# Optimization experiments

Measured on AMD Instinct MI355X. Metric: run time of the kernel, lower is better.

The kernel has to match this reference:

```python
import jax, jax.numpy as jnp
import numpy as np

B, C, T, H, W = 8, 512, 8, 32, 32
CI = C // 2  # inter_channels
EPS = 1e-5


def _conv1x1(x, w, b):
    # x: (b, c, t, h, w); w: (o, c); b: (o,)
    return jnp.einsum('bcthw,oc->bothw', x, w) + b[None, :, None, None, None]


def _maxpool2(v):
    # MaxPool3d(kernel=2, stride=2) on (t, h, w)
    b, c, t, h, w = v.shape
    return v.reshape(b, c, t // 2, 2, h // 2, 2, w // 2, 2).max(axis=(3, 5, 7))


def setup_inputs() -> dict:
    key = jax.random.key(0)
    ks = jax.random.split(key, 12)
    s = 0.02
    return {
        'x': jax.random.normal(ks[0], (B, C, T, H, W), dtype=jnp.float32),
        'theta_w': jax.random.normal(ks[1], (CI, C), dtype=jnp.float32) * s,
        'theta_b': jnp.zeros((CI,), dtype=jnp.float32),
        'phi_w': jax.random.normal(ks[2], (CI, C), dtype=jnp.float32) * s,
        'phi_b': jnp.zeros((CI,), dtype=jnp.float32),
        'g_w': jax.random.normal(ks[3], (CI, C), dtype=jnp.float32) * s,
        'g_b': jnp.zeros((CI,), dtype=jnp.float32),
        'wz_w': jax.random.normal(ks[4], (C, CI), dtype=jnp.float32) * s,
        'wz_b': jnp.zeros((C,), dtype=jnp.float32),
        'bn_gamma': jax.random.uniform(ks[5], (C,), dtype=jnp.float32, minval=0.5, maxval=1.5),
        'bn_beta': jax.random.normal(ks[6], (C,), dtype=jnp.float32) * 0.1,
    }


def reference(x, theta_w, theta_b, phi_w, phi_b, g_w, g_b, wz_w, wz_b, bn_gamma, bn_beta):
    b = x.shape[0]
    # projections (1x1x1 convs == channel matmuls)
    theta_x = _conv1x1(x, theta_w, theta_b)            # (b, ci, t, h, w)
    phi_x = _maxpool2(_conv1x1(x, phi_w, phi_b))       # (b, ci, t/2, h/2, w/2)
    g_x = _maxpool2(_conv1x1(x, g_w, g_b))             # (b, ci, t/2, h/2, w/2)

    ci = theta_x.shape[1]
    q = theta_x.reshape(b, ci, -1).transpose(0, 2, 1)  # (b, N, ci)
    k = phi_x.reshape(b, ci, -1)                       # (b, ci, M)
    v = g_x.reshape(b, ci, -1).transpose(0, 2, 1)      # (b, M, ci)

    f = jnp.einsum('bnc,bcm->bnm', q, k)               # (b, N, M)
    attn = jax.nn.softmax(f, axis=-1)                  # embedded_gaussian
    y = jnp.einsum('bnm,bmc->bnc', attn, v)            # (b, N, ci)
    y = y.transpose(0, 2, 1).reshape(b, ci, *x.shape[2:])

    # Wz: 1x1x1 conv + BatchNorm3d (training-mode batch stats, eps=1e-5)
    z = _conv1x1(y, wz_w, wz_b)                        # (b, C, t, h, w)
    mean = z.mean(axis=(0, 2, 3, 4), keepdims=True)
    var = z.var(axis=(0, 2, 3, 4), keepdims=True)
    z = (z - mean) * jax.lax.rsqrt(var + EPS)
    z = z * bn_gamma[None, :, None, None, None] + bn_beta[None, :, None, None, None]
    return z + x
```

## Files before the change

kernel.cpp:

```cpp
#include <hip/hip_runtime.h>
#include <math.h>

typedef unsigned short u16;
typedef __attribute__((ext_vector_type(8))) _Float16 half8;
typedef __attribute__((ext_vector_type(4))) float f32x4;

#define NS 8192
#define MS 1024
#define CCH 512
#define CI 256
#define O3 768

__device__ __forceinline__ float h2f(u16 u) {
    _Float16 h; *(u16*)&h = u; return (float)h;
}
__device__ __forceinline__ u16 f2h(float f) {
    _Float16 h = (_Float16)f; return *(u16*)&h;
}

__device__ __forceinline__ void gld16(u16* lds, const u16* g) {
    __builtin_amdgcn_global_load_lds((const __attribute__((address_space(1))) void*)g,
                                     (__attribute__((address_space(3))) void*)lds,
                                     16, 0, 0);
}

__global__ void prep_w(const float* __restrict__ tw, const float* __restrict__ tb,
                       const float* __restrict__ pw, const float* __restrict__ pb,
                       const float* __restrict__ gw, const float* __restrict__ gb,
                       const float* __restrict__ wzw,
                       u16* __restrict__ W3b, float* __restrict__ b3, u16* __restrict__ wzb) {
    int i = blockIdx.x * 256 + threadIdx.x;
    if (i < O3 * CCH) {
        int o = i >> 9, c = i & 511;
        float v = (o < 256) ? tw[o * 512 + c] : (o < 512) ? pw[(o - 256) * 512 + c]
                                              : gw[(o - 512) * 512 + c];
        W3b[i] = f2h(v);
    } else {
        int j = i - O3 * CCH;
        if (j < CCH * CI) wzb[j] = f2h(wzw[j]);
    }
    if (i < O3) b3[i] = (i < 256) ? tb[i] : (i < 512) ? pb[i - 256] : gb[i - 512];
}

__global__ __launch_bounds__(256) void transpose_x(const float* __restrict__ x,
                                                   u16* __restrict__ xt) {
    __shared__ float tile[64][129];
    int b = blockIdx.z;
    int n0 = blockIdx.x * 128, c0 = blockIdx.y * 64;
    const float* xb = x + ((size_t)b * CCH + c0) * NS + n0;
    int t = threadIdx.x;
    #pragma unroll
    for (int i = 0; i < 32; ++i) {
        int idx = t + i * 256;
        int c = idx >> 7, n = idx & 127;
        tile[c][n] = xb[(size_t)c * NS + n];
    }
    __syncthreads();
    u16* xo = xt + ((size_t)b * NS + n0) * CCH + c0;
    #pragma unroll
    for (int i = 0; i < 16; ++i) {
        int idx = t + i * 256;
        int cp = idx & 31, n = idx >> 5;
        unsigned lo = f2h(tile[2 * cp][n]);
        unsigned hi = f2h(tile[2 * cp + 1][n]);
        *(unsigned*)(xo + (size_t)n * CCH + 2 * cp) = lo | (hi << 16);
    }
}

template<int BIAS_MODE>
__global__ __launch_bounds__(256) void gemm_nt_f16(
        const u16* __restrict__ A, const u16* __restrict__ Bm,
        u16* __restrict__ C, const float* __restrict__ bias,
        int lda, int ldb, int ldc, int Ksize,
        size_t strideA, size_t strideB, size_t strideC) {
    __shared__ u16 As[128 * 64];
    __shared__ u16 Bs[128 * 64];
    const int t = threadIdx.x;
    const int l = t & 63, w = t >> 6;
    const int wr = w >> 1, wc = w & 1;
    const int fr = l & 15, fq = l >> 4;

    const int nx = gridDim.x, ny = gridDim.y;
    int bid = blockIdx.x + nx * (blockIdx.y + ny * blockIdx.z);
    int cpx = (nx * ny * (int)gridDim.z) >> 3;
    int W = (bid & 7) * cpx + (bid >> 3);
    int bx = W % nx, rem = W / nx;
    int by = rem % ny, bz = rem / ny;

    const u16* gA = A + (size_t)bz * strideA + (size_t)(by * 128) * lda;
    const u16* gB = Bm + (size_t)bz * strideB + (size_t)(bx * 128) * ldb;

    f32x4 acc[4][4];
    #pragma unroll
    for (int m = 0; m < 4; ++m)
        #pragma unroll
        for (int n = 0; n < 4; ++n) acc[m][n] = (f32x4)0.f;

    for (int k0 = 0; k0 < Ksize; k0 += 64) {
        #pragma unroll
        for (int i = 0; i < 4; ++i) {
            int cd = t + i * 256;
            int row = cd >> 3, k8 = (cd & 7) * 8;
            int lbase = (cd & ~63) * 8;
            gld16(&As[lbase], gA + (size_t)row * lda + k0 + k8);
            gld16(&Bs[lbase], gB + (size_t)row * ldb + k0 + k8);
        }
        __syncthreads();

        half8 fa[4][2], fb[4][2];
        #pragma unroll
        for (int m = 0; m < 4; ++m)
            #pragma unroll
            for (int kk = 0; kk < 2; ++kk) {
                fa[m][kk] = *(const half8*)&As[(wr * 64 + m * 16 + fr) * 64 + kk * 32 + fq * 8];
                fb[m][kk] = *(const half8*)&Bs[(wc * 64 + m * 16 + fr) * 64 + kk * 32 + fq * 8];
            }
        #pragma unroll
        for (int kk = 0; kk < 2; ++kk)
            #pragma unroll
            for (int m = 0; m < 4; ++m)
                #pragma unroll
                for (int n = 0; n < 4; ++n)
                    acc[m][n] = __builtin_amdgcn_mfma_f32_16x16x32_f16(
                        fa[m][kk], fb[n][kk], acc[m][n], 0, 0, 0);
        __syncthreads();
    }

    u16* gC = C + (size_t)bz * strideC;
    const int crow0 = by * 128 + wr * 64;
    const int ccol0 = bx * 128 + wc * 64;
    #pragma unroll
    for (int m = 0; m < 4; ++m) {
        #pragma unroll
        for (int n = 0; n < 4; ++n) {
            int col = ccol0 + n * 16 + fr;
            float cb = (BIAS_MODE == 2) ? bias[col] : 0.f;
            #pragma unroll
            for (int j = 0; j < 4; ++j) {
                int row = crow0 + m * 16 + fq * 4 + j;
                float v = acc[m][n][j] + cb;
                if (BIAS_MODE == 1) v += bias[row];
                gC[(size_t)row * ldc + col] = f2h(v);
            }
        }
    }
}

__global__ __launch_bounds__(256) void pool_kernel(const u16* __restrict__ proj,
                                                   u16* __restrict__ kb, u16* __restrict__ vg) {
    int tid = blockIdx.x * 256 + threadIdx.x;
    int b = tid >> 18;
    int m = (tid >> 8) & 1023;
    int ci = tid & 255;
    int tp = m >> 8, hp = (m >> 4) & 15, wp = m & 15;
    const u16* pb = proj + (size_t)b * NS * O3;
    float mk = -1e30f, mv = -1e30f;
    #pragma unroll
    for (int d = 0; d < 8; ++d) {
        int dt = d >> 2, dh = (d >> 1) & 1, dw = d & 1;
        int n = (2 * tp + dt) * 1024 + (2 * hp + dh) * 32 + (2 * wp + dw);
        const u16* r = pb + (size_t)n * O3;
        mk = fmaxf(mk, h2f(r[256 + ci]));
        mv = fmaxf(mv, h2f(r[512 + ci]));
    }
    kb[((size_t)b * MS + m) * CI + ci] = f2h(mk);
    vg[((size_t)b * CI + ci) * MS + m] = f2h(mv);
}

__global__ __launch_bounds__(512, 2) void attn_fused(
        const u16* __restrict__ proj, const u16* __restrict__ kb,
        const u16* __restrict__ vg, u16* __restrict__ y) {
    __shared__ u16 Ks[2][64 * 256];
    __shared__ u16 Vs[2][256 * 64];
    __shared__ u16 Ps[8][16][40];

    int bid0 = blockIdx.x + 64 * blockIdx.y;
    int W = (bid0 & 7) * 64 + (bid0 >> 3);
    const int b = W >> 6;
    const int n0 = (W & 63) * 128;

    const int t = threadIdx.x;
    const int l = t & 63, w = t >> 6;
    const int fr = l & 15, fq = l >> 4;

    const u16* projb = proj + (size_t)b * NS * O3;
    const u16* kbb = kb + (size_t)b * MS * CI;
    const u16* vgb = vg + (size_t)b * CI * MS;

    half8 qf[8];
    {
        const u16* qrow = projb + (size_t)(n0 + w * 16 + fr) * O3 + fq * 8;
        #pragma unroll
        for (int kk = 0; kk < 8; ++kk)
            qf[kk] = *(const half8*)(qrow + kk * 32);
    }

    f32x4 accO[16];
    #pragma unroll
    for (int nf = 0; nf < 16; ++nf) accO[nf] = (f32x4)0.f;
    float m_run[4], l_run[4];
    #pragma unroll
    for (int j = 0; j < 4; ++j) { m_run[j] = -1e30f; l_run[j] = 0.f; }

    #define STAGE_KV(buf, m0)                                                     \
        {                                                                         \
            _Pragma("unroll")                                                     \
            for (int i = 0; i < 4; ++i) {                                         \
                int c = t + i * 512;                                              \
                int lb = (c & ~63) << 3;                                          \
                int krow = c >> 5, kk8 = c & 31;                                  \
                gld16(&Ks[buf][lb],                                               \
                      kbb + (size_t)((m0) + krow) * CI + ((kk8 ^ (krow & 7)) << 3)); \
                int vrow = c >> 3, vk8 = c & 7;                                   \
                gld16(&Vs[buf][lb],                                               \
                      vgb + (size_t)vrow * MS + (m0) + ((vk8 ^ (vrow & 7)) << 3)); \
            }                                                                     \
        }

    STAGE_KV(0, 0);
    STAGE_KV(1, 64);

    for (int mt = 0; mt < 16; ++mt) {
        const int cur = mt & 1;
        if (mt == 15) asm volatile("s_waitcnt vmcnt(0)" ::: "memory");
        else          asm volatile("s_waitcnt vmcnt(8)" ::: "memory");
        __builtin_amdgcn_sched_barrier(0);
        __builtin_amdgcn_s_barrier();

        f32x4 accS[4];
        #pragma unroll
        for (int nf = 0; nf < 4; ++nf) accS[nf] = (f32x4)0.f;
        __builtin_amdgcn_s_setprio(1);
        #pragma unroll
        for (int kk = 0; kk < 8; ++kk) {
            half8 fb[4];
            #pragma unroll
            for (int nf = 0; nf < 4; ++nf) {
                int row = nf * 16 + fr;
                fb[nf] = *(const half8*)&Ks[cur][row * 256 + (((kk << 2) | fq) ^ (row & 7)) * 8];
            }
            #pragma unroll
            for (int nf = 0; nf < 4; ++nf)
                accS[nf] = __builtin_amdgcn_mfma_f32_16x16x32_f16(
                    qf[kk], fb[nf], accS[nf], 0, 0, 0);
        }
        __builtin_amdgcn_s_setprio(0);

        float pm[4];
        #pragma unroll
        for (int j = 0; j < 4; ++j)
            pm[j] = fmaxf(fmaxf(accS[0][j], accS[1][j]),
                          fmaxf(accS[2][j], accS[3][j]));
        #pragma unroll
        for (int off = 1; off < 16; off <<= 1)
            #pragma unroll
            for (int j = 0; j < 4; ++j)
                pm[j] = fmaxf(pm[j], __shfl_xor(pm[j], off));

        int chg = 0;
        #pragma unroll
        for (int j = 0; j < 4; ++j) chg |= (pm[j] > m_run[j]);
        if (__any(chg)) {
            #pragma unroll
            for (int j = 0; j < 4; ++j) {
                float mn = fmaxf(m_run[j], pm[j]);
                float a = __expf(m_run[j] - mn);
                m_run[j] = mn;
                l_run[j] *= a;
                #pragma unroll
                for (int nf = 0; nf < 16; ++nf) accO[nf][j] *= a;
            }
        }

        #pragma unroll
        for (int kkm = 0; kkm < 2; ++kkm) {
            #pragma unroll
            for (int j = 0; j < 4; ++j) {
                float ps = 0.f;
                #pragma unroll
                for (int nfh = 0; nfh < 2; ++nfh) {
                    float p = __expf(accS[kkm * 2 + nfh][j] - m_run[j]);
                    ps += p;
                    Ps[w][fq * 4 + j][nfh * 16 + fr] = f2h(p);
                }
                #pragma unroll
                for (int off = 1; off < 16; off <<= 1) ps += __shfl_xor(ps, off);
                l_run[j] += ps;
            }
            half8 fa = *(const half8*)&Ps[w][fr][fq * 8];
            __builtin_amdgcn_s_setprio(1);
            #pragma unroll
            for (int nf = 0; nf < 16; ++nf) {
                int row = nf * 16 + fr;
                half8 fbv = *(const half8*)&Vs[cur][row * 64 + (((kkm << 2) | fq) ^ (row & 7)) * 8];
                accO[nf] = __builtin_amdgcn_mfma_f32_16x16x32_f16(
                    fa, fbv, accO[nf], 0, 0, 0);
            }
            __builtin_amdgcn_s_setprio(0);
        }

        __builtin_amdgcn_s_barrier();
        if (mt < 14) STAGE_KV(cur, (mt + 2) * 64);
    }

    u16* yb = y + ((size_t)b * NS + n0 + w * 16) * CI;
    #pragma unroll
    for (int j = 0; j < 4; ++j) {
        float inv = 1.f / l_run[j];
        int row = fq * 4 + j;
        #pragma unroll
        for (int nf = 0; nf < 16; ++nf)
            yb[(size_t)row * CI + nf * 16 + fr] = f2h(accO[nf][j] * inv);
    }
    #undef STAGE_KV
}

__global__ __launch_bounds__(256) void bn_stats(const u16* __restrict__ z,
                                                float* __restrict__ stats) {
    int c = blockIdx.x, t = threadIdx.x;
    float s = 0.f, q = 0.f;
    for (int b = 0; b < 8; ++b) {
        const u16* p = z + ((size_t)b * CCH + c) * NS;
        #pragma unroll
        for (int i = 0; i < 4; ++i) {
            uint4 v = *(const uint4*)(p + (t + i * 256) * 8);
            const u16* u = (const u16*)&v;
            #pragma unroll
            for (int j = 0; j < 8; ++j) { float f = h2f(u[j]); s += f; q += f * f; }
        }
    }
    #pragma unroll
    for (int off = 32; off; off >>= 1) { s += __shfl_xor(s, off); q += __shfl_xor(q, off); }
    __shared__ float rs[4], rq[4];
    int w = t >> 6;
    if ((t & 63) == 0) { rs[w] = s; rq[w] = q; }
    __syncthreads();
    if (t == 0) {
        float S2 = rs[0] + rs[1] + rs[2] + rs[3];
        float Q = rq[0] + rq[1] + rq[2] + rq[3];
        const float inv = 1.f / 65536.f;
        float mean = S2 * inv;
        float var = Q * inv - mean * mean;
        stats[c] = mean;
        stats[CCH + c] = rsqrtf(var + 1e-5f);
    }
}

__global__ __launch_bounds__(256) void bn_final(const u16* __restrict__ z,
                                                const float* __restrict__ x,
                                                const float* __restrict__ stats,
                                                const float* __restrict__ gamma,
                                                const float* __restrict__ beta,
                                                float* __restrict__ out) {
    size_t i = ((size_t)blockIdx.x * 256 + threadIdx.x) * 8;
    int c = (int)((i >> 13) & 511);
    float g = gamma[c] * stats[CCH + c];
    float sh = beta[c] - stats[c] * g;
    uint4 zv = *(const uint4*)(z + i);
    const u16* u = (const u16*)&zv;
    float4 x0 = *(const float4*)(x + i);
    float4 x1 = *(const float4*)(x + i + 4);
    float4 o0, o1;
    o0.x = h2f(u[0]) * g + sh + x0.x;
    o0.y = h2f(u[1]) * g + sh + x0.y;
    o0.z = h2f(u[2]) * g + sh + x0.z;
    o0.w = h2f(u[3]) * g + sh + x0.w;
    o1.x = h2f(u[4]) * g + sh + x1.x;
    o1.y = h2f(u[5]) * g + sh + x1.y;
    o1.z = h2f(u[6]) * g + sh + x1.z;
    o1.w = h2f(u[7]) * g + sh + x1.w;
    *(float4*)(out + i) = o0;
    *(float4*)(out + i + 4) = o1;
}

extern "C" void kernel_launch(void* const* d_in, const int* in_sizes, int n_in,
                              void* d_out, int out_size, void* d_ws, size_t ws_size,
                              hipStream_t stream) {
    const float* x       = (const float*)d_in[0];
    const float* theta_w = (const float*)d_in[1];
    const float* theta_b = (const float*)d_in[2];
    const float* phi_w   = (const float*)d_in[3];
    const float* phi_b   = (const float*)d_in[4];
    const float* g_w     = (const float*)d_in[5];
    const float* g_b     = (const float*)d_in[6];
    const float* wz_w    = (const float*)d_in[7];
    const float* wz_b    = (const float*)d_in[8];
    const float* gamma   = (const float*)d_in[9];
    const float* beta    = (const float*)d_in[10];

    char* base = (char*)d_ws;
    u16*   W3b  = (u16*)base;
    float* b3   = (float*)(base + 786432);
    u16*   wzb  = (u16*)(base + 789504);
    float* stats= (float*)(base + 1051648);
    u16* xt   = (u16*)(base + 1056768);
    u16* kb   = xt;
    u16* vg   = xt + (size_t)8 * MS * CI;
    u16* z    = xt;
    u16* proj = (u16*)(base + 1056768 + 67108864);
    u16* y    = (u16*)(base + 1056768 + 67108864 + 100663296);

    prep_w<<<2048, 256, 0, stream>>>(theta_w, theta_b, phi_w, phi_b, g_w, g_b,
                                     wz_w, W3b, b3, wzb);
    transpose_x<<<dim3(64, 8, 8), 256, 0, stream>>>(x, xt);

    gemm_nt_f16<2><<<dim3(6, 64, 8), 256, 0, stream>>>(
        xt, W3b, proj, b3, CCH, CCH, O3, CCH,
        (size_t)NS * CCH, 0, (size_t)NS * O3);

    pool_kernel<<<8192, 256, 0, stream>>>(proj, kb, vg);

    attn_fused<<<dim3(64, 8), 512, 0, stream>>>(proj, kb, vg, y);

    gemm_nt_f16<1><<<dim3(64, 4, 8), 256, 0, stream>>>(
        wzb, y, z, wz_b, CI, CI, NS, CI,
        0, (size_t)NS * CI, (size_t)CCH * NS);

    bn_stats<<<CCH, 256, 0, stream>>>(z, stats);

    bn_final<<<16384, 256, 0, stream>>>(z, x, stats, gamma, beta, (float*)d_out);
}
```

Before: 388.1 us.

## Fuse x transpose/fp16 conversion into projection GEMM and XOR-swizzle LDS tiles

```diff
diff --git a/kernel.cpp b/kernel.cpp
--- a/kernel.cpp
+++ b/kernel.cpp
@@ -42,28 +42,101 @@
     if (i < O3) b3[i] = (i < 256) ? tb[i] : (i < 512) ? pb[i - 256] : gb[i - 512];
 }
 
-__global__ __launch_bounds__(256) void transpose_x(const float* __restrict__ x,
-                                                   u16* __restrict__ xt) {
-    __shared__ float tile[64][129];
-    int b = blockIdx.z;
-    int n0 = blockIdx.x * 128, c0 = blockIdx.y * 64;
-    const float* xb = x + ((size_t)b * CCH + c0) * NS + n0;
-    int t = threadIdx.x;
-    #pragma unroll
-    for (int i = 0; i < 32; ++i) {
-        int idx = t + i * 256;
-        int c = idx >> 7, n = idx & 127;
-        tile[c][n] = xb[(size_t)c * NS + n];
-    }
-    __syncthreads();
-    u16* xo = xt + ((size_t)b * NS + n0) * CCH + c0;
-    #pragma unroll
-    for (int i = 0; i < 16; ++i) {
-        int idx = t + i * 256;
-        int cp = idx & 31, n = idx >> 5;
-        unsigned lo = f2h(tile[2 * cp][n]);
-        unsigned hi = f2h(tile[2 * cp + 1][n]);
-        *(unsigned*)(xo + (size_t)n * CCH + 2 * cp) = lo | (hi << 16);
+__global__ __launch_bounds__(256) void proj_gemm(
+        const float* __restrict__ x, const u16* __restrict__ W3b,
+        const float* __restrict__ b3, u16* __restrict__ proj) {
+    __shared__ float Traw[64][129];
+    __shared__ u16 As[128 * 64];
+    __shared__ u16 Bs[128 * 64];
+    const int t = threadIdx.x;
+    const int l = t & 63, w = t >> 6;
+    const int wr = w >> 1, wc = w & 1;
+    const int fr = l & 15, fq = l >> 4;
+
+    const int nx = gridDim.x, ny = gridDim.y;
+    int bid = blockIdx.x + nx * (blockIdx.y + ny * blockIdx.z);
+    int cpx = (nx * ny * (int)gridDim.z) >> 3;
+    int Wd = (bid & 7) * cpx + (bid >> 3);
+    int bx = Wd % nx, rem = Wd / nx;
+    int by = rem % ny, bz = rem / ny;
+
+    const float* gx = x + (size_t)bz * CCH * NS + by * 128;
+    const u16* gB = W3b + (size_t)(bx * 128) * CCH;
+
+    f32x4 acc[4][4];
+    #pragma unroll
+    for (int m = 0; m < 4; ++m)
+        #pragma unroll
+        for (int n = 0; n < 4; ++n) acc[m][n] = (f32x4)0.f;
+
+    for (int k0 = 0; k0 < CCH; k0 += 64) {
+        #pragma unroll
+        for (int i = 0; i < 4; ++i) {
+            int cd = t + i * 256;
+            int row = cd >> 3;
+            int k8 = ((cd & 7) ^ (row & 7)) * 8;
+            int lbase = (cd & ~63) * 8;
+            gld16(&Bs[lbase], gB + (size_t)row * CCH + k0 + k8);
+        }
+        #pragma unroll
+        for (int i = 0; i < 8; ++i) {
+            int idx = t + i * 256;
+            int c = idx >> 5, nq = idx & 31;
+            float4 v = *(const float4*)(gx + (size_t)(k0 + c) * NS + nq * 4);
+            Traw[c][nq * 4 + 0] = v.x;
+            Traw[c][nq * 4 + 1] = v.y;
+            Traw[c][nq * 4 + 2] = v.z;
+            Traw[c][nq * 4 + 3] = v.w;
+        }
+        __syncthreads();
+        #pragma unroll
+        for (int i = 0; i < 16; ++i) {
+            int idx = t + i * 256;
+            int cp = idx & 31, n = idx >> 5;
+            unsigned lo = f2h(Traw[2 * cp][n]);
+            unsigned hi = f2h(Traw[2 * cp + 1][n]);
+            int chunk = (cp >> 2) ^ (n & 7);
+            *(unsigned*)((char*)As + n * 128 + chunk * 16 + (cp & 3) * 4)
+                = lo | (hi << 16);
+        }
+        __syncthreads();
+
+        half8 fa[4][2], fb[4][2];
+        #pragma unroll
+        for (int m = 0; m < 4; ++m)
+            #pragma unroll
+            for (int kk = 0; kk < 2; ++kk) {
+                int ra = wr * 64 + m * 16 + fr;
+                int rb = wc * 64 + m * 16 + fr;
+                fa[m][kk] = *(const half8*)&As[ra * 64 + ((((kk << 2) | fq)) ^ (ra & 7)) * 8];
+                fb[m][kk] = *(const half8*)&Bs[rb * 64 + ((((kk << 2) | fq)) ^ (rb & 7)) * 8];
+            }
+        #pragma unroll
+        for (int kk = 0; kk < 2; ++kk)
+            #pragma unroll
+            for (int m = 0; m < 4; ++m)
+                #pragma unroll
+                for (int n = 0; n < 4; ++n)
+                    acc[m][n] = __builtin_amdgcn_mfma_f32_16x16x32_f16(
+                        fa[m][kk], fb[n][kk], acc[m][n], 0, 0, 0);
+        __syncthreads();
+    }
+
+    u16* gC = proj + (size_t)bz * NS * O3;
+    const int crow0 = by * 128 + wr * 64;
+    const int ccol0 = bx * 128 + wc * 64;
+    #pragma unroll
+    for (int m = 0; m < 4; ++m) {
+        #pragma unroll
+        for (int n = 0; n < 4; ++n) {
+            int col = ccol0 + n * 16 + fr;
+            float cb = b3[col];
+            #pragma unroll
+            for (int j = 0; j < 4; ++j) {
+                int row = crow0 + m * 16 + fq * 4 + j;
+                gC[(size_t)row * O3 + col] = f2h(acc[m][n][j] + cb);
+            }
+        }
     }
 }
 
@@ -83,8 +156,8 @@
     const int nx = gridDim.x, ny = gridDim.y;
     int bid = blockIdx.x + nx * (blockIdx.y + ny * blockIdx.z);
     int cpx = (nx * ny * (int)gridDim.z) >> 3;
-    int W = (bid & 7) * cpx + (bid >> 3);
-    int bx = W % nx, rem = W / nx;
+    int Wd = (bid & 7) * cpx + (bid >> 3);
+    int bx = Wd % nx, rem = Wd / nx;
     int by = rem % ny, bz = rem / ny;
 
     const u16* gA = A + (size_t)bz * strideA + (size_t)(by * 128) * lda;
@@ -100,7 +173,8 @@
         #pragma unroll
         for (int i = 0; i < 4; ++i) {
             int cd = t + i * 256;
-            int row = cd >> 3, k8 = (cd & 7) * 8;
+            int row = cd >> 3;
+            int k8 = ((cd & 7) ^ (row & 7)) * 8;
             int lbase = (cd & ~63) * 8;
             gld16(&As[lbase], gA + (size_t)row * lda + k0 + k8);
             gld16(&Bs[lbase], gB + (size_t)row * ldb + k0 + k8);
@@ -112,8 +186,10 @@
         for (int m = 0; m < 4; ++m)
             #pragma unroll
             for (int kk = 0; kk < 2; ++kk) {
-                fa[m][kk] = *(const half8*)&As[(wr * 64 + m * 16 + fr) * 64 + kk * 32 + fq * 8];
-                fb[m][kk] = *(const half8*)&Bs[(wc * 64 + m * 16 + fr) * 64 + kk * 32 + fq * 8];
+                int ra = wr * 64 + m * 16 + fr;
+                int rb = wc * 64 + m * 16 + fr;
+                fa[m][kk] = *(const half8*)&As[ra * 64 + ((((kk << 2) | fq)) ^ (ra & 7)) * 8];
+                fb[m][kk] = *(const half8*)&Bs[rb * 64 + ((((kk << 2) | fq)) ^ (rb & 7)) * 8];
             }
         #pragma unroll
         for (int kk = 0; kk < 2; ++kk)
@@ -393,20 +469,16 @@
     float* b3   = (float*)(base + 786432);
     u16*   wzb  = (u16*)(base + 789504);
     float* stats= (float*)(base + 1051648);
-    u16* xt   = (u16*)(base + 1056768);
-    u16* kb   = xt;
-    u16* vg   = xt + (size_t)8 * MS * CI;
-    u16* z    = xt;
+    u16* kb   = (u16*)(base + 1056768);
+    u16* vg   = kb + (size_t)8 * MS * CI;
+    u16* z    = kb;
     u16* proj = (u16*)(base + 1056768 + 67108864);
     u16* y    = (u16*)(base + 1056768 + 67108864 + 100663296);
 
     prep_w<<<2048, 256, 0, stream>>>(theta_w, theta_b, phi_w, phi_b, g_w, g_b,
                                      wz_w, W3b, b3, wzb);
-    transpose_x<<<dim3(64, 8, 8), 256, 0, stream>>>(x, xt);
-
-    gemm_nt_f16<2><<<dim3(6, 64, 8), 256, 0, stream>>>(
-        xt, W3b, proj, b3, CCH, CCH, O3, CCH,
-        (size_t)NS * CCH, 0, (size_t)NS * O3);
+
+    proj_gemm<<<dim3(6, 64, 8), 256, 0, stream>>>(x, W3b, b3, proj);
 
     pool_kernel<<<8192, 256, 0, stream>>>(proj, kb, vg);
 
```

Measured after the change: 426.5 us. 1.1x slower.

## Double-buffer GEMM LDS tiles with async prefetch and XOR swizzle

Applied to the files above, without the earlier changes.

```diff
diff --git a/kernel.cpp b/kernel.cpp
--- a/kernel.cpp
+++ b/kernel.cpp
@@ -73,8 +73,8 @@
         u16* __restrict__ C, const float* __restrict__ bias,
         int lda, int ldb, int ldc, int Ksize,
         size_t strideA, size_t strideB, size_t strideC) {
-    __shared__ u16 As[128 * 64];
-    __shared__ u16 Bs[128 * 64];
+    __shared__ u16 As[2][128 * 64];
+    __shared__ u16 Bs[2][128 * 64];
     const int t = threadIdx.x;
     const int l = t & 63, w = t >> 6;
     const int wr = w >> 1, wc = w & 1;
@@ -83,8 +83,8 @@
     const int nx = gridDim.x, ny = gridDim.y;
     int bid = blockIdx.x + nx * (blockIdx.y + ny * blockIdx.z);
     int cpx = (nx * ny * (int)gridDim.z) >> 3;
-    int W = (bid & 7) * cpx + (bid >> 3);
-    int bx = W % nx, rem = W / nx;
+    int Wd = (bid & 7) * cpx + (bid >> 3);
+    int bx = Wd % nx, rem = Wd / nx;
     int by = rem % ny, bz = rem / ny;
 
     const u16* gA = A + (size_t)bz * strideA + (size_t)(by * 128) * lda;
@@ -96,25 +96,41 @@
         #pragma unroll
         for (int n = 0; n < 4; ++n) acc[m][n] = (f32x4)0.f;
 
-    for (int k0 = 0; k0 < Ksize; k0 += 64) {
-        #pragma unroll
-        for (int i = 0; i < 4; ++i) {
-            int cd = t + i * 256;
-            int row = cd >> 3, k8 = (cd & 7) * 8;
-            int lbase = (cd & ~63) * 8;
-            gld16(&As[lbase], gA + (size_t)row * lda + k0 + k8);
-            gld16(&Bs[lbase], gB + (size_t)row * ldb + k0 + k8);
-        }
-        __syncthreads();
+    #define STAGE_AB(buf, k0)                                                 \
+        {                                                                     \
+            _Pragma("unroll")                                                 \
+            for (int i = 0; i < 4; ++i) {                                     \
+                int cd = t + i * 256;                                         \
+                int row = cd >> 3;                                            \
+                int k8 = ((cd & 7) ^ (row & 7)) * 8;                          \
+                int lbase = (cd & ~63) * 8;                                   \
+                gld16(&As[buf][lbase], gA + (size_t)row * lda + (k0) + k8);   \
+                gld16(&Bs[buf][lbase], gB + (size_t)row * ldb + (k0) + k8);   \
+            }                                                                 \
+        }
+
+    const int nk = Ksize >> 6;
+    STAGE_AB(0, 0);
+    STAGE_AB(1, 64);
+
+    for (int mt = 0; mt < nk; ++mt) {
+        const int cur = mt & 1;
+        if (mt == nk - 1) asm volatile("s_waitcnt vmcnt(0)" ::: "memory");
+        else              asm volatile("s_waitcnt vmcnt(8)" ::: "memory");
+        __builtin_amdgcn_sched_barrier(0);
+        __builtin_amdgcn_s_barrier();
 
         half8 fa[4][2], fb[4][2];
         #pragma unroll
         for (int m = 0; m < 4; ++m)
             #pragma unroll
             for (int kk = 0; kk < 2; ++kk) {
-                fa[m][kk] = *(const half8*)&As[(wr * 64 + m * 16 + fr) * 64 + kk * 32 + fq * 8];
-                fb[m][kk] = *(const half8*)&Bs[(wc * 64 + m * 16 + fr) * 64 + kk * 32 + fq * 8];
-            }
+                int ra = wr * 64 + m * 16 + fr;
+                int rb = wc * 64 + m * 16 + fr;
+                fa[m][kk] = *(const half8*)&As[cur][ra * 64 + ((((kk << 2) | fq)) ^ (ra & 7)) * 8];
+                fb[m][kk] = *(const half8*)&Bs[cur][rb * 64 + ((((kk << 2) | fq)) ^ (rb & 7)) * 8];
+            }
+        __builtin_amdgcn_s_setprio(1);
         #pragma unroll
         for (int kk = 0; kk < 2; ++kk)
             #pragma unroll
@@ -123,8 +139,12 @@
                 for (int n = 0; n < 4; ++n)
                     acc[m][n] = __builtin_amdgcn_mfma_f32_16x16x32_f16(
                         fa[m][kk], fb[n][kk], acc[m][n], 0, 0, 0);
-        __syncthreads();
-    }
+        __builtin_amdgcn_s_setprio(0);
+
+        __builtin_amdgcn_s_barrier();
+        if (mt + 2 < nk) STAGE_AB(cur, (mt + 2) * 64);
+    }
+    #undef STAGE_AB
 
     u16* gC = C + (size_t)bz * strideC;
     const int crow0 = by * 128 + wr * 64;
```

Measured after the change: 383.2 us. Within noise of the previous version (-1.3%).
